# Kernel optimization log

Measured on AMD Instinct MI355X. Metric: run time of the kernel, lower is better.

Reference implementation:

```python
import jax, jax.numpy as jnp
import numpy as np

P_DIMS = [100, 100, 80, 60, 60]
P = sum(P_DIMS)  # 400
N_STREAMS = len(P_DIMS)
MEM_ITERS = 5
DECAY = 0.8
LR = 0.5        # hebbian_learning_rate
FORGET = 0.9999 # hebbian_forget_rate
NEG_SLOPE = 0.01


def _build_masks():
    idx = np.cumsum([0] + P_DIMS)
    hier = np.zeros((P, P), np.float32)
    for i in range(N_STREAMS):
        for j in range(i, N_STREAMS):
            hier[idx[i]:idx[i + 1], idx[j]:idx[j + 1]] = 1.0
    iters = [MEM_ITERS - f for f in range(N_STREAMS)]  # [5,4,3,2,1]
    rmasks = np.zeros((MEM_ITERS, P), np.float32)
    for it in range(MEM_ITERS):
        for s, r in enumerate(iters):
            if it < r:
                rmasks[it, idx[s]:idx[s + 1]] = 1.0
    return jnp.asarray(hier), jnp.asarray(rmasks)


def setup_inputs() -> dict:
    key = jax.random.key(0)
    k1, k2, k3, k4 = jax.random.split(key, 4)
    B = 512
    return {
        'M_prev': jax.random.normal(k1, (B, P, P), dtype=jnp.float32) * 0.1,
        'p_inferred': jax.random.normal(k2, (B, P), dtype=jnp.float32),
        'p_generated': jax.random.normal(k3, (B, P), dtype=jnp.float32),
        'query': jax.random.normal(k4, (B, P), dtype=jnp.float32),
    }


def reference(M_prev, p_inferred, p_generated, query):
    hier_mask, retrieval_masks = _build_masks()

    # Hebbian update: M = clamp(forget*M_prev + lr*(p-phat)(p+phat)^T, -1, 1) * hier_mask
    outer = (p_inferred - p_generated)[:, :, None] * (p_inferred + p_generated)[:, None, :]
    M = jnp.clip(FORGET * M_prev + LR * outer, -1.0, 1.0) * hier_mask

    # Hierarchical attractor retrieval
    h = jax.nn.leaky_relu(jnp.clip(query, -1.0, 1.0), NEG_SLOPE)

    def step(h, mask):
        mv = jnp.einsum('bpq,bq->bp', M, h)
        upd = jax.nn.leaky_relu(jnp.clip(DECAY * h + mv, -1.0, 1.0), NEG_SLOPE)
        return (1.0 - mask) * h + mask * upd, None

    h, _ = jax.lax.scan(step, h, retrieval_masks)
    return h
```

## Files before the change

### kernel.cpp

```cpp
#include <hip/hip_runtime.h>


#define PDIM 400
#define RREG 4
#define LROW0 32
#define LROWN 78
#define FORGET 0.9999f
#define LRATE  0.5f
#define DECAY  0.8f
#define SLOPE  0.01f

typedef float f32x2 __attribute__((ext_vector_type(2)));
union V4 { float4 f4; f32x2 h2[2]; };

__device__ __forceinline__ float leaky_clip(float x) {
    x = fminf(fmaxf(x, -1.0f), 1.0f);
    return x > 0.0f ? x : SLOPE * x;
}
__device__ __forceinline__ float clamp1(float x) {
    return fminf(fmaxf(x, -1.0f), 1.0f);
}
__device__ __forceinline__ f32x2 pk_mul(f32x2 a, f32x2 b) {
    f32x2 d;
    asm("v_pk_mul_f32 %0, %1, %2" : "=v"(d) : "v"(a), "v"(b));
    return d;
}
__device__ __forceinline__ f32x2 pk_fma(f32x2 a, f32x2 b, f32x2 c) {
    f32x2 d;
    asm("v_pk_fma_f32 %0, %1, %2, %3" : "=v"(d) : "v"(a), "v"(b), "v"(c));
    return d;
}
__device__ __forceinline__ f32x2 clamp2(f32x2 x) {
    x.x = clamp1(x.x); x.y = clamp1(x.y); return x;
}

__device__ __forceinline__ int c4beg(int p) {
    return (p < 100) ? 0 : (p < 200) ? 25 : (p < 280) ? 50 : (p < 340) ? 70 : 85;
}

__device__ __forceinline__ float wave_sum(float x) {
    x += __int_as_float(__builtin_amdgcn_update_dpp(0, __float_as_int(x), 0xB1,  0xf, 0xf, true));
    x += __int_as_float(__builtin_amdgcn_update_dpp(0, __float_as_int(x), 0x4E,  0xf, 0xf, true));
    x += __int_as_float(__builtin_amdgcn_update_dpp(0, __float_as_int(x), 0x141, 0xf, 0xf, true));
    x += __int_as_float(__builtin_amdgcn_update_dpp(0, __float_as_int(x), 0x140, 0xf, 0xf, true));
    x += __int_as_float(__builtin_amdgcn_update_dpp(0, __float_as_int(x), 0x142, 0xf, 0xf, true));
    x += __int_as_float(__builtin_amdgcn_update_dpp(0, __float_as_int(x), 0x143, 0xf, 0xf, true));
    return __int_as_float(__builtin_amdgcn_readlane(__float_as_int(x), 63));
}

__device__ __forceinline__ void load_row(const float* __restrict__ Mb,
                                         int p, int R, int l,
                                         int& c4, V4& A, V4& B) {
    A.f4 = make_float4(0.f, 0.f, 0.f, 0.f);
    B.f4 = A.f4;
    c4 = 0;
    if (p < R) {
        c4 = c4beg(p);
        const float* __restrict__ row = Mb + (size_t)p * PDIM;
        if (l >= c4)                A.f4 = *(const float4*)(row + 4 * l);
        if (l < 36 && 64 + l >= c4) B.f4 = *(const float4*)(row + 256 + 4 * l);
    }
}

__global__ __launch_bounds__(512, 4)
void hier_mem_kernel(const float* __restrict__ M_prev,
                     const float* __restrict__ p_inf,
                     const float* __restrict__ p_gen,
                     const float* __restrict__ query,
                     float* __restrict__ out)
{
    __shared__ float s_mc[LROWN - LROW0][PDIM];
    __shared__ float s_h[2][PDIM];
    __shared__ float s_la[PDIM];

    const int b   = blockIdx.x;
    const int tid = threadIdx.x;
    const int l   = tid & 63;
    const int wid = tid >> 6;
    const float* __restrict__ Mb = M_prev + (size_t)b * PDIM * PDIM;

    if (tid < PDIM) {
        const float pi = p_inf[b * PDIM + tid];
        const float pg = p_gen[b * PDIM + tid];
        s_la[tid]   = LRATE * (pi - pg);
        s_h[0][tid] = leaky_clip(query[b * PDIM + tid]);
    }

    const float4 z4 = make_float4(0.f, 0.f, 0.f, 0.f);
    const float4* __restrict__ pi4 = (const float4*)(p_inf + (size_t)b * PDIM);
    const float4* __restrict__ pg4 = (const float4*)(p_gen + (size_t)b * PDIM);
    V4 vA, vB; vB.f4 = z4;
    {
        const float4 x = pi4[l], y = pg4[l];
        vA.f4 = make_float4(x.x + y.x, x.y + y.y, x.z + y.z, x.w + y.w);
        if (l < 36) {
            const float4 u = pi4[64 + l], v = pg4[64 + l];
            vB.f4 = make_float4(u.x + v.x, u.y + v.y, u.z + v.z, u.w + v.w);
        }
    }
    const f32x2 F2 = {FORGET, FORGET};

    V4 rA[RREG], rB[RREG];

    __syncthreads();

    {
        const float* __restrict__ hcur = s_h[0];
        float* __restrict__ hnew = s_h[1];
        V4 hA, hB; hB.f4 = z4;
        hA.f4 = *(const float4*)(hcur + 4 * l);
        if (l < 36) hB.f4 = *(const float4*)(hcur + 256 + 4 * l);

        int p = wid;
        int c0, c1; V4 A0, B0, A1, B1;
        load_row(Mb, p,     PDIM, l, c0, A0, B0);
        load_row(Mb, p + 8, PDIM, l, c1, A1, B1);

        #pragma unroll
        for (int k = 0; k < RREG; ++k) {
            int c2; V4 A2, B2;
            load_row(Mb, p + 16, PDIM, l, c2, A2, B2);

            const float la = s_la[p];
            const f32x2 la2 = {la, la};
            V4 mA, mB; mA.f4 = z4; mB.f4 = z4;
            mA.h2[0] = clamp2(pk_fma(F2, A0.h2[0], pk_mul(la2, vA.h2[0])));
            mA.h2[1] = clamp2(pk_fma(F2, A0.h2[1], pk_mul(la2, vA.h2[1])));
            if (l < 36) {
                mB.h2[0] = clamp2(pk_fma(F2, B0.h2[0], pk_mul(la2, vB.h2[0])));
                mB.h2[1] = clamp2(pk_fma(F2, B0.h2[1], pk_mul(la2, vB.h2[1])));
            }
            rA[k] = mA; rB[k] = mB;

            f32x2 acc2 = pk_fma(mA.h2[0], hA.h2[0],
                         pk_fma(mA.h2[1], hA.h2[1],
                         pk_fma(mB.h2[0], hB.h2[0],
                         pk_mul(mB.h2[1], hB.h2[1]))));
            const float tot = wave_sum(acc2.x + acc2.y);
            if (l == 0) {
                hnew[p] = leaky_clip(fmaf(DECAY, hcur[p], tot));
            }
            p += 8; c0 = c1; A0 = A1; B0 = B1; c1 = c2; A1 = A2; B1 = B2;
        }

        while (p < PDIM) {
            int c2; V4 A2, B2;
            load_row(Mb, p + 16, PDIM, l, c2, A2, B2);

            const float la = s_la[p];
            const f32x2 la2 = {la, la};
            f32x2 acc2 = {0.f, 0.f};
            V4 mA, mB; mA.f4 = z4; mB.f4 = z4;
            if (l >= c0) {
                mA.h2[0] = clamp2(pk_fma(F2, A0.h2[0], pk_mul(la2, vA.h2[0])));
                mA.h2[1] = clamp2(pk_fma(F2, A0.h2[1], pk_mul(la2, vA.h2[1])));
                acc2 = pk_fma(mA.h2[0], hA.h2[0], acc2);
                acc2 = pk_fma(mA.h2[1], hA.h2[1], acc2);
            }
            if (l < 36 && 64 + l >= c0) {
                mB.h2[0] = clamp2(pk_fma(F2, B0.h2[0], pk_mul(la2, vB.h2[0])));
                mB.h2[1] = clamp2(pk_fma(F2, B0.h2[1], pk_mul(la2, vB.h2[1])));
                acc2 = pk_fma(mB.h2[0], hB.h2[0], acc2);
                acc2 = pk_fma(mB.h2[1], hB.h2[1], acc2);
            }
            if (p < LROWN) {
                *(float4*)&s_mc[p - LROW0][4 * l] = mA.f4;
                if (l < 36) *(float4*)&s_mc[p - LROW0][256 + 4 * l] = mB.f4;
            }

            const float tot = wave_sum(acc2.x + acc2.y);
            if (l == 0) {
                hnew[p] = leaky_clip(fmaf(DECAY, hcur[p], tot));
            }

            p += 8; c0 = c1; A0 = A1; B0 = B1; c1 = c2; A1 = A2; B1 = B2;
        }
        __syncthreads();
    }

    int cur = 1;
    const int Rt[4] = {340, 280, 200, 100};
    #pragma unroll
    for (int t = 0; t < 4; ++t) {
        const int R = Rt[t];
        const float* __restrict__ hcur = s_h[cur];
        float* __restrict__ hnew = s_h[cur ^ 1];

        V4 hA, hB; hB.f4 = z4;
        hA.f4 = *(const float4*)(hcur + 4 * l);
        if (l < 36) hB.f4 = *(const float4*)(hcur + 256 + 4 * l);

        int sp = LROWN + wid;
        int c0, c1; V4 A0, B0, A1, B1;
        load_row(Mb, sp,     R, l, c0, A0, B0);
        load_row(Mb, sp + 8, R, l, c1, A1, B1);

        #pragma unroll
        for (int k = 0; k < RREG; ++k) {
            const int p = wid + 8 * k;
            f32x2 acc2 = pk_fma(rA[k].h2[0], hA.h2[0],
                         pk_fma(rA[k].h2[1], hA.h2[1],
                         pk_fma(rB[k].h2[0], hB.h2[0],
                         pk_mul(rB[k].h2[1], hB.h2[1]))));
            const float tot = wave_sum(acc2.x + acc2.y);
            if (l == 0) {
                hnew[p] = leaky_clip(fmaf(DECAY, hcur[p], tot));
            }
        }

        {
            int p = LROW0 + wid;
            V4 KA, KB; KB.f4 = z4;
            KA.f4 = *(const float4*)&s_mc[p - LROW0][4 * l];
            if (l < 36) KB.f4 = *(const float4*)&s_mc[p - LROW0][256 + 4 * l];
            while (p < LROWN) {
                const int pn = p + 8;
                V4 NA, NB; NA.f4 = z4; NB.f4 = z4;
                if (pn < LROWN) {
                    NA.f4 = *(const float4*)&s_mc[pn - LROW0][4 * l];
                    if (l < 36) NB.f4 = *(const float4*)&s_mc[pn - LROW0][256 + 4 * l];
                }
                f32x2 acc2 = pk_fma(KA.h2[0], hA.h2[0],
                             pk_fma(KA.h2[1], hA.h2[1],
                             pk_fma(KB.h2[0], hB.h2[0],
                             pk_mul(KB.h2[1], hB.h2[1]))));
                const float tot = wave_sum(acc2.x + acc2.y);
                if (l == 0) {
                    hnew[p] = leaky_clip(fmaf(DECAY, hcur[p], tot));
                }
                p = pn; KA = NA; KB = NB;
            }
        }

        while (sp < R) {
            int c2; V4 A2, B2;
            load_row(Mb, sp + 16, R, l, c2, A2, B2);

            const float la = s_la[sp];
            const f32x2 la2 = {la, la};
            f32x2 acc2 = {0.f, 0.f};
            if (l >= c0) {
                f32x2 m0 = clamp2(pk_fma(F2, A0.h2[0], pk_mul(la2, vA.h2[0])));
                f32x2 m1 = clamp2(pk_fma(F2, A0.h2[1], pk_mul(la2, vA.h2[1])));
                acc2 = pk_fma(m0, hA.h2[0], acc2);
                acc2 = pk_fma(m1, hA.h2[1], acc2);
            }
            if (l < 36 && 64 + l >= c0) {
                f32x2 m0 = clamp2(pk_fma(F2, B0.h2[0], pk_mul(la2, vB.h2[0])));
                f32x2 m1 = clamp2(pk_fma(F2, B0.h2[1], pk_mul(la2, vB.h2[1])));
                acc2 = pk_fma(m0, hB.h2[0], acc2);
                acc2 = pk_fma(m1, hB.h2[1], acc2);
            }

            const float tot = wave_sum(acc2.x + acc2.y);
            if (l == 0) {
                hnew[sp] = leaky_clip(fmaf(DECAY, hcur[sp], tot));
            }

            sp += 8; c0 = c1; A0 = A1; B0 = B1; c1 = c2; A1 = A2; B1 = B2;
        }

        if (tid >= R && tid < PDIM) hnew[tid] = hcur[tid];
        __syncthreads();
        cur ^= 1;
    }

    if (tid < PDIM) {
        out[b * PDIM + tid] = s_h[cur][tid];
    }
}

extern "C" void kernel_launch(void* const* d_in, const int* in_sizes, int n_in,
                              void* d_out, int out_size, void* d_ws, size_t ws_size,
                              hipStream_t stream) {
    const float* M_prev = (const float*)d_in[0];
    const float* p_inf  = (const float*)d_in[1];
    const float* p_gen  = (const float*)d_in[2];
    const float* query  = (const float*)d_in[3];
    float* out = (float*)d_out;

    const int B = in_sizes[1] / PDIM;
    hipLaunchKernelGGL(hier_mem_kernel, dim3(B), dim3(512), 0, stream,
                       M_prev, p_inf, p_gen, query, out);
}
```

Measured before the change: 473.5 us.

## Cache frozen-column partial sums to skip reloading M columns in later iterations

In the later retrieval iterations, the contribution of columns whose h entries are already frozen is accumulated once into a per-row shared buffer (s_C). Later passes then load and recompute only the still-active column range of each M row, cutting global memory traffic for the tail rows. The wave reduction also drops the final readlane and lets lane 63 write the result. The cost is a second wave reduction in the folding passes, plus extra shared-memory reads and writes and more per-lane predicates.

```diff
diff --git a/kernel.cpp b/kernel.cpp
--- a/kernel.cpp
+++ b/kernel.cpp
@@ -5,6 +5,7 @@
 #define RREG 4
 #define LROW0 32
 #define LROWN 78
+#define TAIL0 78
 #define FORGET 0.9999f
 #define LRATE  0.5f
 #define DECAY  0.8f
@@ -30,6 +31,11 @@
     asm("v_pk_fma_f32 %0, %1, %2, %3" : "=v"(d) : "v"(a), "v"(b), "v"(c));
     return d;
 }
+__device__ __forceinline__ f32x2 pk_add(f32x2 a, f32x2 b) {
+    f32x2 d;
+    asm("v_pk_add_f32 %0, %1, %2" : "=v"(d) : "v"(a), "v"(b));
+    return d;
+}
 __device__ __forceinline__ f32x2 clamp2(f32x2 x) {
     x.x = clamp1(x.x); x.y = clamp1(x.y); return x;
 }
@@ -38,27 +44,28 @@
     return (p < 100) ? 0 : (p < 200) ? 25 : (p < 280) ? 50 : (p < 340) ? 70 : 85;
 }
 
-__device__ __forceinline__ float wave_sum(float x) {
+__device__ __forceinline__ float wave_red63(float x) {
     x += __int_as_float(__builtin_amdgcn_update_dpp(0, __float_as_int(x), 0xB1,  0xf, 0xf, true));
     x += __int_as_float(__builtin_amdgcn_update_dpp(0, __float_as_int(x), 0x4E,  0xf, 0xf, true));
     x += __int_as_float(__builtin_amdgcn_update_dpp(0, __float_as_int(x), 0x141, 0xf, 0xf, true));
     x += __int_as_float(__builtin_amdgcn_update_dpp(0, __float_as_int(x), 0x140, 0xf, 0xf, true));
     x += __int_as_float(__builtin_amdgcn_update_dpp(0, __float_as_int(x), 0x142, 0xf, 0xf, true));
     x += __int_as_float(__builtin_amdgcn_update_dpp(0, __float_as_int(x), 0x143, 0xf, 0xf, true));
-    return __int_as_float(__builtin_amdgcn_readlane(__float_as_int(x), 63));
-}
-
-__device__ __forceinline__ void load_row(const float* __restrict__ Mb,
-                                         int p, int R, int l,
-                                         int& c4, V4& A, V4& B) {
+    return x;
+}
+
+__device__ __forceinline__ void load_row_lim(const float* __restrict__ Mb,
+                                             int p, int R, int l, int CPREV,
+                                             int& c4, V4& A, V4& B) {
     A.f4 = make_float4(0.f, 0.f, 0.f, 0.f);
     B.f4 = A.f4;
     c4 = 0;
+    const int blim = (CPREV >= 100) ? 36 : (CPREV > 64 ? CPREV - 64 : 0);
     if (p < R) {
         c4 = c4beg(p);
         const float* __restrict__ row = Mb + (size_t)p * PDIM;
-        if (l >= c4)                A.f4 = *(const float4*)(row + 4 * l);
-        if (l < 36 && 64 + l >= c4) B.f4 = *(const float4*)(row + 256 + 4 * l);
+        if (l >= c4 && l < CPREV)    A.f4 = *(const float4*)(row + 4 * l);
+        if (l < blim && 64 + l >= c4) B.f4 = *(const float4*)(row + 256 + 4 * l);
     }
 }
 
@@ -72,6 +79,7 @@
     __shared__ float s_mc[LROWN - LROW0][PDIM];
     __shared__ float s_h[2][PDIM];
     __shared__ float s_la[PDIM];
+    __shared__ float s_C[PDIM];
 
     const int b   = blockIdx.x;
     const int tid = threadIdx.x;
@@ -84,6 +92,7 @@
         const float pg = p_gen[b * PDIM + tid];
         s_la[tid]   = LRATE * (pi - pg);
         s_h[0][tid] = leaky_clip(query[b * PDIM + tid]);
+        s_C[tid]    = 0.f;
     }
 
     const float4 z4 = make_float4(0.f, 0.f, 0.f, 0.f);
@@ -113,13 +122,13 @@
 
         int p = wid;
         int c0, c1; V4 A0, B0, A1, B1;
-        load_row(Mb, p,     PDIM, l, c0, A0, B0);
-        load_row(Mb, p + 8, PDIM, l, c1, A1, B1);
+        load_row_lim(Mb, p,     PDIM, l, 100, c0, A0, B0);
+        load_row_lim(Mb, p + 8, PDIM, l, 100, c1, A1, B1);
 
         #pragma unroll
         for (int k = 0; k < RREG; ++k) {
             int c2; V4 A2, B2;
-            load_row(Mb, p + 16, PDIM, l, c2, A2, B2);
+            load_row_lim(Mb, p + 16, PDIM, l, 100, c2, A2, B2);
 
             const float la = s_la[p];
             const f32x2 la2 = {la, la};
@@ -136,8 +145,8 @@
                          pk_fma(mA.h2[1], hA.h2[1],
                          pk_fma(mB.h2[0], hB.h2[0],
                          pk_mul(mB.h2[1], hB.h2[1]))));
-            const float tot = wave_sum(acc2.x + acc2.y);
-            if (l == 0) {
+            const float tot = wave_red63(acc2.x + acc2.y);
+            if (l == 63) {
                 hnew[p] = leaky_clip(fmaf(DECAY, hcur[p], tot));
             }
             p += 8; c0 = c1; A0 = A1; B0 = B1; c1 = c2; A1 = A2; B1 = B2;
@@ -145,7 +154,7 @@
 
         while (p < PDIM) {
             int c2; V4 A2, B2;
-            load_row(Mb, p + 16, PDIM, l, c2, A2, B2);
+            load_row_lim(Mb, p + 16, PDIM, l, 100, c2, A2, B2);
 
             const float la = s_la[p];
             const f32x2 la2 = {la, la};
@@ -168,8 +177,8 @@
                 if (l < 36) *(float4*)&s_mc[p - LROW0][256 + 4 * l] = mB.f4;
             }
 
-            const float tot = wave_sum(acc2.x + acc2.y);
-            if (l == 0) {
+            const float tot = wave_red63(acc2.x + acc2.y);
+            if (l == 63) {
                 hnew[p] = leaky_clip(fmaf(DECAY, hcur[p], tot));
             }
 
@@ -179,10 +188,24 @@
     }
 
     int cur = 1;
-    const int Rt[4] = {340, 280, 200, 100};
+    const int Rt[4]    = {340, 280, 200, 100};
+    const int CPREVt[4]= {100,  85,  70,  50};
+    const int CCURt[4] = { 85,  70,  50, 100};
+    const int BLIMt[4] = { 36,  21,   6,   0};
+    const int BACTt[4] = { 21,   6,   0,   0};
+    const int FOLDt[4] = {  1,   1,   1,   0};
+    const int PSURVt[4]= {280, 200, 100,   0};
+
     #pragma unroll
     for (int t = 0; t < 4; ++t) {
-        const int R = Rt[t];
+        const int R     = Rt[t];
+        const int CPREV = CPREVt[t];
+        const int CCUR  = CCURt[t];
+        const int BLIM  = BLIMt[t];
+        const int BACT  = BACTt[t];
+        const int FOLD  = FOLDt[t];
+        const int PSURV = PSURVt[t];
+
         const float* __restrict__ hcur = s_h[cur];
         float* __restrict__ hnew = s_h[cur ^ 1];
 
@@ -190,10 +213,10 @@
         hA.f4 = *(const float4*)(hcur + 4 * l);
         if (l < 36) hB.f4 = *(const float4*)(hcur + 256 + 4 * l);
 
-        int sp = LROWN + wid;
+        int sp = TAIL0 + wid;
         int c0, c1; V4 A0, B0, A1, B1;
-        load_row(Mb, sp,     R, l, c0, A0, B0);
-        load_row(Mb, sp + 8, R, l, c1, A1, B1);
+        load_row_lim(Mb, sp,     R, l, CPREV, c0, A0, B0);
+        load_row_lim(Mb, sp + 8, R, l, CPREV, c1, A1, B1);
 
         #pragma unroll
         for (int k = 0; k < RREG; ++k) {
@@ -202,8 +225,8 @@
                          pk_fma(rA[k].h2[1], hA.h2[1],
                          pk_fma(rB[k].h2[0], hB.h2[0],
                          pk_mul(rB[k].h2[1], hB.h2[1]))));
-            const float tot = wave_sum(acc2.x + acc2.y);
-            if (l == 0) {
+            const float tot = wave_red63(acc2.x + acc2.y);
+            if (l == 63) {
                 hnew[p] = leaky_clip(fmaf(DECAY, hcur[p], tot));
             }
         }
@@ -224,8 +247,8 @@
                              pk_fma(KA.h2[1], hA.h2[1],
                              pk_fma(KB.h2[0], hB.h2[0],
                              pk_mul(KB.h2[1], hB.h2[1]))));
-                const float tot = wave_sum(acc2.x + acc2.y);
-                if (l == 0) {
+                const float tot = wave_red63(acc2.x + acc2.y);
+                if (l == 63) {
                     hnew[p] = leaky_clip(fmaf(DECAY, hcur[p], tot));
                 }
                 p = pn; KA = NA; KB = NB;
@@ -234,27 +257,34 @@
 
         while (sp < R) {
             int c2; V4 A2, B2;
-            load_row(Mb, sp + 16, R, l, c2, A2, B2);
+            load_row_lim(Mb, sp + 16, R, l, CPREV, c2, A2, B2);
 
             const float la = s_la[sp];
             const f32x2 la2 = {la, la};
-            f32x2 acc2 = {0.f, 0.f};
-            if (l >= c0) {
+            f32x2 accA = {0.f, 0.f};
+            f32x2 accB = {0.f, 0.f};
+            if (l >= c0 && l < CPREV) {
                 f32x2 m0 = clamp2(pk_fma(F2, A0.h2[0], pk_mul(la2, vA.h2[0])));
                 f32x2 m1 = clamp2(pk_fma(F2, A0.h2[1], pk_mul(la2, vA.h2[1])));
-                acc2 = pk_fma(m0, hA.h2[0], acc2);
-                acc2 = pk_fma(m1, hA.h2[1], acc2);
-            }
-            if (l < 36 && 64 + l >= c0) {
+                f32x2 d  = pk_fma(m0, hA.h2[0], pk_mul(m1, hA.h2[1]));
+                if (CCUR >= 64 || l < CCUR) accA = pk_add(accA, d);
+                else                        accB = pk_add(accB, d);
+            }
+            if (l < BLIM && 64 + l >= c0) {
                 f32x2 m0 = clamp2(pk_fma(F2, B0.h2[0], pk_mul(la2, vB.h2[0])));
                 f32x2 m1 = clamp2(pk_fma(F2, B0.h2[1], pk_mul(la2, vB.h2[1])));
-                acc2 = pk_fma(m0, hB.h2[0], acc2);
-                acc2 = pk_fma(m1, hB.h2[1], acc2);
-            }
-
-            const float tot = wave_sum(acc2.x + acc2.y);
-            if (l == 0) {
-                hnew[sp] = leaky_clip(fmaf(DECAY, hcur[sp], tot));
+                f32x2 d  = pk_fma(m0, hB.h2[0], pk_mul(m1, hB.h2[1]));
+                if (l < BACT) accA = pk_add(accA, d);
+                else          accB = pk_add(accB, d);
+            }
+
+            const float ta = wave_red63(accA.x + accA.y);
+            float tb = 0.f;
+            if (FOLD) tb = wave_red63(accB.x + accB.y);
+            if (l == 63) {
+                const float Cp = s_C[sp];
+                if (FOLD && sp < PSURV) s_C[sp] = Cp + tb;
+                hnew[sp] = leaky_clip(fmaf(DECAY, hcur[sp], ta + tb + Cp));
             }
 
             sp += 8; c0 = c1; A0 = A1; B0 = B1; c1 = c2; A1 = A2; B1 = B2;
```

Measured after the change: 478.8 us. Within noise of the previous version (+1.1%).
